# Performance work log

Measured on AMD Instinct MI355X. Metric: run time of the kernel, lower is better.

## Reference

```python
import math
import jax, jax.numpy as jnp
import numpy as np

B, C, H, W, ATTR = 4, 1024, 16, 8, 21

def setup_inputs() -> dict:
    key = jax.random.key(0)
    ks = jax.random.split(key, 7)
    rn = lambda k, shape, s=1.0: jax.random.normal(k, shape, dtype=jnp.float32) * s
    return {
        "feature": rn(ks[0], (B, C, H, W)),
        "Q": rn(ks[1], (B, C, ATTR)),                 # self.Q parameter
        "W1": rn(ks[2], (C, C), 0.02),                # conv1x1 linear_1 weight [out,in]
        "b1": jnp.zeros((C,), jnp.float32),
        "W2": rn(ks[3], (C, C), 0.02),                # conv1x1 linear_2 weight
        "b2": jnp.zeros((C,), jnp.float32),
        "W3": rn(ks[4], (ATTR * C, ATTR * C), 0.005), # linear_3 weight (bias=False)
        "fc_w": rn(ks[5], (1, C), 0.02),              # fc weight
        "fc_b": jnp.zeros((1,), jnp.float32),
    }

def reference(feature, Q, W1, b1, W2, b2, W3, fc_w, fc_b):
    b, c, h, w = feature.shape
    attr = Q.shape[-1]
    f = feature.reshape(b, c, h * w)                      # [b,c,n]
    # 1x1 convs == per-pixel linear over channels
    lf1 = jnp.einsum('oc,bcn->bon', W1, f) + b1[None, :, None]
    lf2 = jnp.einsum('oc,bcn->bon', W2, f) + b2[None, :, None]
    # linear_3 on flattened self.Q (nn.Linear: x @ W.T)
    lq = (Q.reshape(b, -1) @ W3.T).reshape(b, c, attr)    # [b,c,attr]
    Qp = jnp.transpose(lq, (0, 2, 1))                      # [b,attr,c]
    QK = jnp.einsum('bic,bcn->bin', Qp, lf1) / math.sqrt(c)  # [b,attr,n]
    A = jax.nn.softmax(QK, axis=1)                         # softmax over attr dim (dim=1, as in torch)
    ff = jnp.einsum('bin,bcn->bic', A, lf2)                # [b,attr,c]
    # NOTE: the original loops ssca_forward head_num=3 times, but ssca_forward
    # ignores its Q argument (always reads self.Q), so all 3 iterations produce
    # the identical tensor; one pass is mathematically equivalent.
    pred = (ff @ fc_w.T + fc_b)[..., 0]                    # [b,attr]
    return pred
```

## Files before the change

kernel.cpp:

```cpp
#include <hip/hip_runtime.h>

#define K3   21504
#define C_   1024
#define NPIX 128
#define NATTR 21
#define NB   4

typedef float f32x4 __attribute__((ext_vector_type(4)));

__device__ __forceinline__ float wave_reduce_sum(float v) {
  #pragma unroll
  for (int off = 32; off > 0; off >>= 1)
    v += __shfl_xor(v, off, 64);
  return v;
}


#define LOAD_TILE(W_, Q_, kk)                                          \
  {                                                                    \
    _Pragma("unroll")                                                  \
    for (int r = 0; r < 4; ++r) {                                      \
      const float* rp = r0 + (size_t)r * K3 + (kk);                    \
      W_[r][0] = __builtin_nontemporal_load((const f32x4*)rp);         \
      W_[r][1] = __builtin_nontemporal_load((const f32x4*)(rp + 256)); \
    }                                                                  \
    _Pragma("unroll")                                                  \
    for (int b = 0; b < NB; ++b) {                                     \
      const float* qp = Q + (size_t)b * K3 + (kk);                     \
      Q_[b][0] = *(const f32x4*)qp;                                    \
      Q_[b][1] = *(const f32x4*)(qp + 256);                            \
    }                                                                  \
  }

#define FMA_TILE(W_, Q_)                                               \
  {                                                                    \
    _Pragma("unroll")                                                  \
    for (int r = 0; r < 4; ++r)                                        \
      _Pragma("unroll")                                                \
      for (int b = 0; b < NB; ++b) {                                   \
        _Pragma("unroll")                                              \
        for (int e = 0; e < 4; ++e) {                                  \
          acc[r][b] += W_[r][0][e] * Q_[b][0][e];                      \
          acc[r][b] += W_[r][1][e] * Q_[b][1][e];                      \
        }                                                              \
      }                                                                \
  }

__global__ __launch_bounds__(64) void k_lq(
    const float* __restrict__ Q, const float* __restrict__ W3,
    float* __restrict__ lq) {
  const int lane = threadIdx.x;
  const int o0 = blockIdx.x * 4;
  const float* r0 = W3 + (size_t)o0 * K3;
  float acc[4][NB];
  #pragma unroll
  for (int r = 0; r < 4; ++r)
    #pragma unroll
    for (int b = 0; b < NB; ++b) acc[r][b] = 0.f;

  f32x4 wA[4][2], qA[NB][2], wB[4][2], qB[NB][2];
  int k = lane * 4;
  LOAD_TILE(wA, qA, k);
  #pragma unroll 1
  for (int it = 0; it < 20; ++it) {
    LOAD_TILE(wB, qB, k + 512);
    FMA_TILE(wA, qA);
    LOAD_TILE(wA, qA, k + 1024);
    FMA_TILE(wB, qB);
    k += 1024;
  }
  LOAD_TILE(wB, qB, k + 512);
  FMA_TILE(wA, qA);
  FMA_TILE(wB, qB);

  #pragma unroll
  for (int r = 0; r < 4; ++r)
    #pragma unroll
    for (int b = 0; b < NB; ++b) {
      float s = wave_reduce_sum(acc[r][b]);
      if (lane == 0) lq[(size_t)b * K3 + o0 + r] = s;
    }
}

__global__ __launch_bounds__(64) void k_d(
    const float* __restrict__ lq, const float* __restrict__ b1,
    const float* __restrict__ b2, const float* __restrict__ fc_w,
    float* __restrict__ dc) {
  const int job = blockIdx.x;
  const int lane = threadIdx.x;
  float acc = 0.f;
  if (job < NB * NATTR) {
    const int b = job / NATTR, i = job % NATTR;
    for (int c = lane; c < C_; c += 64)
      acc += lq[(size_t)b * K3 + c * NATTR + i] * b1[c];
  } else {
    for (int c = lane; c < C_; c += 64)
      acc += fc_w[c] * b2[c];
  }
  acc = wave_reduce_sum(acc);
  if (lane == 0) dc[job] = acc;
}

__global__ __launch_bounds__(256) void k_vu(
    const float* __restrict__ W1, const float* __restrict__ W2,
    const float* __restrict__ lq, const float* __restrict__ fc_w,
    float* __restrict__ vu) {
  const int job = blockIdx.x >> 4;
  const int kc  = blockIdx.x & 15;
  const int cg  = threadIdx.x >> 6;
  const int kl  = threadIdx.x & 63;
  const int k   = kc * 64 + kl;
  const float* M;
  const float* coef;
  int cstride;
  if (job < NB * NATTR) {
    M = W1;
    coef = lq + (size_t)(job / NATTR) * K3 + (job % NATTR);
    cstride = NATTR;
  } else {
    M = W2;
    coef = fc_w;
    cstride = 1;
  }
  float acc = 0.f;
  const int c0 = cg * 256;
  #pragma unroll 8
  for (int c = c0; c < c0 + 256; ++c)
    acc += coef[c * cstride] * M[(size_t)c * C_ + k];
  __shared__ float red[4][64];
  red[cg][kl] = acc;
  __syncthreads();
  if (threadIdx.x < 64) {
    float s = red[0][kl] + red[1][kl] + red[2][kl] + red[3][kl];
    vu[(size_t)job * C_ + k] = s;
  }
}

__global__ __launch_bounds__(256) void k_attn(
    const float* __restrict__ f, const float* __restrict__ vu,
    const float* __restrict__ dc, float* __restrict__ P) {
  const int b = blockIdx.x >> 7;
  const int n = blockIdx.x & 127;
  const int t = threadIdx.x;
  const int wave = t >> 6, lane = t & 63;
  __shared__ float xs[C_];
  __shared__ float red[22][4];
  #pragma unroll
  for (int j = 0; j < 4; ++j) {
    int c = t + j * 256;
    xs[c] = f[((size_t)b * C_ + c) * NPIX + n];
  }
  __syncthreads();
  for (int ii = 0; ii < 22; ++ii) {
    const float* vec = vu + (size_t)((ii < NATTR) ? (b * NATTR + ii) : NB * NATTR) * C_;
    float p = 0.f;
    #pragma unroll
    for (int j = 0; j < 4; ++j) {
      int c = t + j * 256;
      p += xs[c] * vec[c];
    }
    p = wave_reduce_sum(p);
    if (lane == 0) red[ii][wave] = p;
  }
  __syncthreads();
  if (t == 0) {
    float qk[NATTR];
    float m = -1e30f;
    #pragma unroll
    for (int i = 0; i < NATTR; ++i) {
      qk[i] = (red[i][0] + red[i][1] + red[i][2] + red[i][3]
               + dc[b * NATTR + i]) * 0.03125f;
      m = fmaxf(m, qk[i]);
    }
    float g = red[21][0] + red[21][1] + red[21][2] + red[21][3] + dc[NB * NATTR];
    float s = 0.f;
    #pragma unroll
    for (int i = 0; i < NATTR; ++i) { qk[i] = expf(qk[i] - m); s += qk[i]; }
    const float inv = g / s;
    #pragma unroll
    for (int i = 0; i < NATTR; ++i)
      P[(size_t)(b * NATTR + i) * NPIX + n] = qk[i] * inv;
  }
}

__global__ __launch_bounds__(64) void k_pred(
    const float* __restrict__ P, const float* __restrict__ fc_b,
    float* __restrict__ out) {
  const int job = blockIdx.x;
  const int lane = threadIdx.x;
  float acc = P[(size_t)job * NPIX + lane] + P[(size_t)job * NPIX + 64 + lane];
  acc = wave_reduce_sum(acc);
  if (lane == 0) out[job] = acc + fc_b[0];
}

extern "C" void kernel_launch(void* const* d_in, const int* in_sizes, int n_in,
                              void* d_out, int out_size, void* d_ws, size_t ws_size,
                              hipStream_t stream) {
  const float* feature = (const float*)d_in[0];
  const float* Q   = (const float*)d_in[1];
  const float* W1  = (const float*)d_in[2];
  const float* b1  = (const float*)d_in[3];
  const float* W2  = (const float*)d_in[4];
  const float* b2  = (const float*)d_in[5];
  const float* W3  = (const float*)d_in[6];
  const float* fcw = (const float*)d_in[7];
  const float* fcb = (const float*)d_in[8];
  float* out = (float*)d_out;

  float* ws = (float*)d_ws;
  float* lq = ws;
  float* vu = lq + NB * K3;
  float* dc = vu + 85 * C_;
  float* P  = dc + 85;

  hipLaunchKernelGGL(k_lq,   dim3(K3 / 4), dim3(64),  0, stream, Q, W3, lq);
  hipLaunchKernelGGL(k_d,    dim3(85),     dim3(64),  0, stream, lq, b1, b2, fcw, dc);
  hipLaunchKernelGGL(k_vu,   dim3(85 * 16), dim3(256), 0, stream, W1, W2, lq, fcw, vu);
  hipLaunchKernelGGL(k_attn, dim3(NB * NPIX), dim3(256), 0, stream, feature, vu, dc, P);
  hipLaunchKernelGGL(k_pred, dim3(NB * NATTR), dim3(64), 0, stream, P, fcb, out);
}
```

Before: 385.3 us.

## Fuse bias-dot and pred kernels, accumulate output atomically, halve lq rows per block

Folds the dc bias-dot job into extra blocks of k_vu, together with the output initialisation to fc_b. k_pred is removed: k_attn now atomically adds each attention-weighted term straight into the output. This cuts two kernel launches and the P round trip through memory. k_lq now handles 2 rows per block instead of 4, doubling the grid for the dominant W3 streaming at the cost of more Q reloads. The atomics make the summation order nondeterministic.

After: 488.1 us. 26.7% more time.

```diff
diff --git a/kernel.cpp b/kernel.cpp
--- a/kernel.cpp
+++ b/kernel.cpp
@@ -5,6 +5,7 @@
 #define NPIX 128
 #define NATTR 21
 #define NB   4
+#define ROWS 2
 
 typedef float f32x4 __attribute__((ext_vector_type(4)));
 
@@ -19,7 +20,7 @@
 #define LOAD_TILE(W_, Q_, kk)                                          \
   {                                                                    \
     _Pragma("unroll")                                                  \
-    for (int r = 0; r < 4; ++r) {                                      \
+    for (int r = 0; r < ROWS; ++r) {                                   \
       const float* rp = r0 + (size_t)r * K3 + (kk);                    \
       W_[r][0] = __builtin_nontemporal_load((const f32x4*)rp);         \
       W_[r][1] = __builtin_nontemporal_load((const f32x4*)(rp + 256)); \
@@ -35,7 +36,7 @@
 #define FMA_TILE(W_, Q_)                                               \
   {                                                                    \
     _Pragma("unroll")                                                  \
-    for (int r = 0; r < 4; ++r)                                        \
+    for (int r = 0; r < ROWS; ++r)                                     \
       _Pragma("unroll")                                                \
       for (int b = 0; b < NB; ++b) {                                   \
         _Pragma("unroll")                                              \
@@ -50,15 +51,15 @@
     const float* __restrict__ Q, const float* __restrict__ W3,
     float* __restrict__ lq) {
   const int lane = threadIdx.x;
-  const int o0 = blockIdx.x * 4;
+  const int o0 = blockIdx.x * ROWS;
   const float* r0 = W3 + (size_t)o0 * K3;
-  float acc[4][NB];
-  #pragma unroll
-  for (int r = 0; r < 4; ++r)
+  float acc[ROWS][NB];
+  #pragma unroll
+  for (int r = 0; r < ROWS; ++r)
     #pragma unroll
     for (int b = 0; b < NB; ++b) acc[r][b] = 0.f;
 
-  f32x4 wA[4][2], qA[NB][2], wB[4][2], qB[NB][2];
+  f32x4 wA[ROWS][2], qA[NB][2], wB[ROWS][2], qB[NB][2];
   int k = lane * 4;
   LOAD_TILE(wA, qA, k);
   #pragma unroll 1
@@ -74,7 +75,7 @@
   FMA_TILE(wB, qB);
 
   #pragma unroll
-  for (int r = 0; r < 4; ++r)
+  for (int r = 0; r < ROWS; ++r)
     #pragma unroll
     for (int b = 0; b < NB; ++b) {
       float s = wave_reduce_sum(acc[r][b]);
@@ -82,31 +83,38 @@
     }
 }
 
-__global__ __launch_bounds__(64) void k_d(
-    const float* __restrict__ lq, const float* __restrict__ b1,
-    const float* __restrict__ b2, const float* __restrict__ fc_w,
-    float* __restrict__ dc) {
-  const int job = blockIdx.x;
-  const int lane = threadIdx.x;
-  float acc = 0.f;
-  if (job < NB * NATTR) {
-    const int b = job / NATTR, i = job % NATTR;
-    for (int c = lane; c < C_; c += 64)
-      acc += lq[(size_t)b * K3 + c * NATTR + i] * b1[c];
-  } else {
-    for (int c = lane; c < C_; c += 64)
-      acc += fc_w[c] * b2[c];
-  }
-  acc = wave_reduce_sum(acc);
-  if (lane == 0) dc[job] = acc;
-}
-
 __global__ __launch_bounds__(256) void k_vu(
     const float* __restrict__ W1, const float* __restrict__ W2,
     const float* __restrict__ lq, const float* __restrict__ fc_w,
-    float* __restrict__ vu) {
-  const int job = blockIdx.x >> 4;
-  const int kc  = blockIdx.x & 15;
+    const float* __restrict__ b1, const float* __restrict__ b2,
+    const float* __restrict__ fc_b,
+    float* __restrict__ vu, float* __restrict__ dc,
+    float* __restrict__ out) {
+  const int blk = blockIdx.x;
+  if (blk >= 85 * 16) {
+    const int xjob = blk - 85 * 16;
+    if (xjob < 85) {
+      if (threadIdx.x < 64) {
+        const int lane = threadIdx.x;
+        float acc = 0.f;
+        if (xjob < NB * NATTR) {
+          const int b = xjob / NATTR, i = xjob % NATTR;
+          for (int c = lane; c < C_; c += 64)
+            acc += lq[(size_t)b * K3 + c * NATTR + i] * b1[c];
+        } else {
+          for (int c = lane; c < C_; c += 64)
+            acc += fc_w[c] * b2[c];
+        }
+        acc = wave_reduce_sum(acc);
+        if (lane == 0) dc[xjob] = acc;
+      }
+    } else {
+      if (threadIdx.x < NB * NATTR) out[threadIdx.x] = fc_b[0];
+    }
+    return;
+  }
+  const int job = blk >> 4;
+  const int kc  = blk & 15;
   const int cg  = threadIdx.x >> 6;
   const int kl  = threadIdx.x & 63;
   const int k   = kc * 64 + kl;
@@ -138,7 +146,7 @@
 
 __global__ __launch_bounds__(256) void k_attn(
     const float* __restrict__ f, const float* __restrict__ vu,
-    const float* __restrict__ dc, float* __restrict__ P) {
+    const float* __restrict__ dc, float* __restrict__ out) {
   const int b = blockIdx.x >> 7;
   const int n = blockIdx.x & 127;
   const int t = threadIdx.x;
@@ -179,18 +187,8 @@
     const float inv = g / s;
     #pragma unroll
     for (int i = 0; i < NATTR; ++i)
-      P[(size_t)(b * NATTR + i) * NPIX + n] = qk[i] * inv;
-  }
-}
-
-__global__ __launch_bounds__(64) void k_pred(
-    const float* __restrict__ P, const float* __restrict__ fc_b,
-    float* __restrict__ out) {
-  const int job = blockIdx.x;
-  const int lane = threadIdx.x;
-  float acc = P[(size_t)job * NPIX + lane] + P[(size_t)job * NPIX + 64 + lane];
-  acc = wave_reduce_sum(acc);
-  if (lane == 0) out[job] = acc + fc_b[0];
+      atomicAdd(out + b * NATTR + i, qk[i] * inv);
+  }
 }
 
 extern "C" void kernel_launch(void* const* d_in, const int* in_sizes, int n_in,
@@ -211,11 +209,10 @@
   float* lq = ws;
   float* vu = lq + NB * K3;
   float* dc = vu + 85 * C_;
-  float* P  = dc + 85;
-
-  hipLaunchKernelGGL(k_lq,   dim3(K3 / 4), dim3(64),  0, stream, Q, W3, lq);
-  hipLaunchKernelGGL(k_d,    dim3(85),     dim3(64),  0, stream, lq, b1, b2, fcw, dc);
-  hipLaunchKernelGGL(k_vu,   dim3(85 * 16), dim3(256), 0, stream, W1, W2, lq, fcw, vu);
-  hipLaunchKernelGGL(k_attn, dim3(NB * NPIX), dim3(256), 0, stream, feature, vu, dc, P);
-  hipLaunchKernelGGL(k_pred, dim3(NB * NATTR), dim3(64), 0, stream, P, fcb, out);
-}
+
+  hipLaunchKernelGGL(k_lq,   dim3(K3 / ROWS), dim3(64), 0, stream, Q, W3, lq);
+  hipLaunchKernelGGL(k_vu,   dim3(85 * 16 + 86), dim3(256), 0, stream,
+                     W1, W2, lq, fcw, b1, b2, fcb, vu, dc, out);
+  hipLaunchKernelGGL(k_attn, dim3(NB * NPIX), dim3(256), 0, stream,
+                     feature, vu, dc, out);
+}
```
